# Optimization experiments

Hardware: AMD Instinct MI355X
Metric: run time of the kernel (lower is better)

The kernel has to match this reference:

```python
import jax, jax.numpy as jnp
import numpy as np

B_SZ, L, D_MODEL = 8, 4096, 64
D_INNER, D_STATE, DT_RANK, K = 128, 16, 4, 4  # expand=2, d_state=16, dt_rank=ceil(64/16), d_conv=4


def setup_inputs() -> dict:
    key = jax.random.key(0)
    ks = jax.random.split(key, 8)
    r = lambda k, sh, s=0.02: jax.random.normal(k, sh, dtype=jnp.float32) * s
    A_init = jnp.log(jnp.arange(1, D_STATE + 1, dtype=jnp.float32))  # S4D-real init
    return {
        "x": jax.random.normal(ks[0], (B_SZ, L, D_MODEL), dtype=jnp.float32),
        "ln_g": jnp.ones((D_MODEL,), jnp.float32),
        "ln_b": jnp.zeros((D_MODEL,), jnp.float32),
        "in_proj_w": r(ks[1], (2, 2 * D_INNER, D_MODEL)),
        "conv_w": r(ks[2], (2, D_INNER, K), 0.1),
        "conv_b": jnp.zeros((2, D_INNER), jnp.float32),
        "x_proj_w": r(ks[3], (2, DT_RANK + 2 * D_STATE, D_INNER)),
        "dt_proj_w": r(ks[4], (2, D_INNER, DT_RANK), 0.1),
        "dt_bias": jnp.full((2, D_INNER), -4.0, jnp.float32) + r(ks[5], (2, D_INNER), 0.1),
        "A_log": jnp.broadcast_to(A_init, (2, D_INNER, D_STATE)) + 0.0,
        "D": jnp.ones((2, D_INNER), jnp.float32),
        "out_proj_w": r(ks[6], (2, D_MODEL, D_INNER)),
    }


def _mamba(x, in_w, cw, cb, xp_w, dtp_w, dtb, A_log, Dp, out_w):
    # x: [B, L, d_model] -> [B, L, d_model]
    xz = x @ in_w.T                         # [B, L, 2*d_inner]
    xi, z = jnp.split(xz, 2, axis=-1)
    # causal depthwise conv1d, kernel K, left-pad K-1
    xi_c = jnp.transpose(xi, (0, 2, 1))     # [B, d_inner, L]
    xi_c = jax.lax.conv_general_dilated(
        xi_c, cw[:, None, :], (1,), [(K - 1, 0)],
        dimension_numbers=("NCH", "OIH", "NCH"), feature_group_count=D_INNER)
    xi = jax.nn.silu(jnp.transpose(xi_c, (0, 2, 1)) + cb)  # [B, L, d_inner]
    xdb = xi @ xp_w.T                       # [B, L, dt_rank + 2*N]
    dt_low, Bm, C = jnp.split(xdb, [DT_RANK, DT_RANK + D_STATE], axis=-1)
    dt = jax.nn.softplus(dt_low @ dtp_w.T + dtb)  # [B, L, d_inner]
    A = -jnp.exp(A_log)                     # [d_inner, N]

    def step(h, inp):
        xt, dtt, Bt, Ct = inp               # [B,d], [B,d], [B,N], [B,N]
        dA = jnp.exp(dtt[..., None] * A)    # [B, d, N]
        h = dA * h + (dtt * xt)[..., None] * Bt[:, None, :]
        return h, jnp.einsum("bdn,bn->bd", h, Ct)

    h0 = jnp.zeros((x.shape[0], D_INNER, D_STATE), x.dtype)
    seq = (jnp.swapaxes(xi, 0, 1), jnp.swapaxes(dt, 0, 1),
           jnp.swapaxes(Bm, 0, 1), jnp.swapaxes(C, 0, 1))
    _, ys = jax.lax.scan(step, h0, seq)
    y = jnp.swapaxes(ys, 0, 1) + xi * Dp    # D skip connection
    y = y * jax.nn.silu(z)                  # gate
    return y @ out_w.T                      # [B, L, d_model]


def reference(x, ln_g, ln_b, in_proj_w, conv_w, conv_b, x_proj_w, dt_proj_w, dt_bias, A_log, D, out_proj_w):
    mu = jnp.mean(x, axis=-1, keepdims=True)
    var = jnp.var(x, axis=-1, keepdims=True)
    xn = (x - mu) * jax.lax.rsqrt(var + 1e-5) * ln_g + ln_b
    p = lambda i: (in_proj_w[i], conv_w[i], conv_b[i], x_proj_w[i], dt_proj_w[i],
                   dt_bias[i], A_log[i], D[i], out_proj_w[i])
    y_fwd = _mamba(xn, *p(0))
    y_bwd = jnp.flip(_mamba(jnp.flip(xn, axis=1), *p(1)), axis=1)
    return y_fwd + y_bwd
```

## Files before the change

### kernel.cpp

```cpp
#include <hip/hip_runtime.h>

#define Bsz 8
#define Lx 4096
#define DM 64
#define DI 128
#define NS 16
#define RK 4
#define KC 4
#define NC 64
#define CT 64

typedef __attribute__((ext_vector_type(8))) __bf16 bf16x8v;
typedef __attribute__((ext_vector_type(4))) __bf16 bf16x4v;
typedef __attribute__((ext_vector_type(4))) float f32x4;

__device__ __forceinline__ float fsig(float x){ return 1.f/(1.f+__expf(-x)); }
__device__ __forceinline__ float dot4(float4 a, float4 b){
  return fmaf(a.x,b.x, fmaf(a.y,b.y, fmaf(a.z,b.z, a.w*b.w)));
}

__global__ __launch_bounds__(512) void a1_front(
    const float* __restrict__ x, const float* __restrict__ ln_g, const float* __restrict__ ln_b,
    const float* __restrict__ in_w, const float* __restrict__ conv_w, const float* __restrict__ conv_b,
    const float* __restrict__ xp_w, const float* __restrict__ dtp_w, const float* __restrict__ dt_b,
    float* __restrict__ xcg, float* __restrict__ dtg, float* __restrict__ zg,
    float* __restrict__ Bg, float* __restrict__ Cg)
{
  __shared__ float uA[4864];
  __shared__ float uB[8192];
  const int tid = threadIdx.x;
  const int bx = blockIdx.x;
  const int tile = bx & 63;
  const int i = (bx >> 6) & 1;
  const int b = bx >> 7;
  const int l0 = tile * 64;
  const size_t rbase = (size_t)(b*2+i)*Lx + l0;

  {
    const int wv8 = tid >> 6, lane = tid & 63;
    const float gg = ln_g[lane], bb = ln_b[lane];
    for (int lr = wv8; lr < 67; lr += 8) {
      float v = 0.f;
      int l = l0 - 3 + lr;
      if (l >= 0) {
        int pl = i ? (Lx-1-l) : l;
        v = x[((size_t)b*Lx + pl)*DM + lane];
        float s = v, s2 = v*v;
        #pragma unroll
        for (int off=32; off; off>>=1){ s += __shfl_xor(s,off); s2 += __shfl_xor(s2,off); }
        float mu = s * (1.f/DM);
        float rs = rsqrtf(s2*(1.f/DM) - mu*mu + 1e-5f);
        v = (v-mu)*rs*gg + bb;
      }
      *(__bf16*)((char*)uA + ((lr*128 + lane*2) ^ ((lr&7)<<4))) = (__bf16)v;
    }
    #pragma unroll
    for (int it=0; it<8; ++it) {
      int g = it*512 + tid;
      int c = g >> 4, q = g & 15;
      float4 w = *(const float4*)(in_w + ((size_t)(i*2*DI) + c)*DM + q*4);
      bf16x4v hv;
      hv[0]=(__bf16)w.x; hv[1]=(__bf16)w.y; hv[2]=(__bf16)w.z; hv[3]=(__bf16)w.w;
      *(bf16x4v*)((char*)uB + ((c*128 + q*8) ^ ((c&7)<<4))) = hv;
    }
  }
  __syncthreads();

  const int lane = tid & 63, wv = tid >> 6;
  f32x4 acc[5][2];
  {
    f32x4 z4 = {0.f, 0.f, 0.f, 0.f};
    #pragma unroll
    for (int mt=0; mt<5; ++mt){ acc[mt][0] = z4; acc[mt][1] = z4; }
    bf16x8v bfr[2][2];
    #pragma unroll
    for (int ntl=0; ntl<2; ++ntl)
      #pragma unroll
      for (int kt=0; kt<2; ++kt){
        int c = (wv*2+ntl)*16 + (lane&15);
        int byt = (c*128 + kt*64 + (lane>>4)*16) ^ ((c&7)<<4);
        bfr[ntl][kt] = *(const bf16x8v*)((const char*)uB + byt);
      }
    #pragma unroll
    for (int mt=0; mt<5; ++mt){
      bf16x8v afr[2];
      #pragma unroll
      for (int kt=0; kt<2; ++kt){
        int row = mt*16 + (lane&15);
        int byt = (row*128 + kt*64 + (lane>>4)*16) ^ ((row&7)<<4);
        afr[kt] = *(const bf16x8v*)((const char*)uA + byt);
      }
      #pragma unroll
      for (int ntl=0; ntl<2; ++ntl){
        acc[mt][ntl] = __builtin_amdgcn_mfma_f32_16x16x32_bf16(afr[0], bfr[ntl][0], acc[mt][ntl], 0,0,0);
        acc[mt][ntl] = __builtin_amdgcn_mfma_f32_16x16x32_bf16(afr[1], bfr[ntl][1], acc[mt][ntl], 0,0,0);
      }
    }
  }
  __syncthreads();

  {
    const int d = tid & 127, rh = tid >> 7;
    const float4 cw = *(const float4*)(conv_w + (size_t)(i*DI + d)*KC);
    const float cb = conv_b[i*DI + d];
    #pragma unroll
    for (int h=0; h<2; ++h) {
      if (wv < 4) {
        #pragma unroll
        for (int mt=0; mt<5; ++mt)
          #pragma unroll
          for (int ntl=0; ntl<2; ++ntl)
            #pragma unroll
            for (int r=0; r<4; ++r){
              int m = mt*16 + (lane>>4)*4 + r;
              if (m >= h*32 && m <= h*32+34)
                uA[(m - h*32)*129 + wv*32 + ntl*16 + (lane&15)] = acc[mt][ntl][r];
            }
      } else if (h == 0) {
        #pragma unroll
        for (int mt=0; mt<5; ++mt)
          #pragma unroll
          for (int ntl=0; ntl<2; ++ntl)
            #pragma unroll
            for (int r=0; r<4; ++r){
              int m = mt*16 + (lane>>4)*4 + r;
              if (m >= 3 && m <= 66)
                zg[(rbase + (m-3))*DI + (wv-4)*32 + ntl*16 + (lane&15)] = acc[mt][ntl][r];
            }
      }
      __syncthreads();
      #pragma unroll
      for (int rr=0; rr<8; ++rr){
        int r = h*32 + rh*8 + rr;
        int lb = rh*8 + rr;
        float v0 = uA[(lb  )*129 + d];
        float v1 = uA[(lb+1)*129 + d];
        float v2 = uA[(lb+2)*129 + d];
        float v3 = uA[(lb+3)*129 + d];
        float aa = cb + cw.x*v0 + cw.y*v1 + cw.z*v2 + cw.w*v3;
        float xc = aa * fsig(aa);
        xcg[(rbase + r)*DI + d] = xc;
        __bf16 hh = (__bf16)xc;
        __bf16 ll = (__bf16)(xc - (float)hh);
        int off = (r*256 + d*2) ^ ((r&7)<<4);
        *(__bf16*)((char*)uB + off) = hh;
        *(__bf16*)((char*)uB + off + 16384) = ll;
      }
      __syncthreads();
    }
  }

  for (int e = tid; e < 36*32; e += 512) {
    int j = e >> 5, k0 = (e & 31)*4;
    float4 w = *(const float4*)(xp_w + ((size_t)(i*36) + j)*DI + k0);
    float vv[4] = {w.x, w.y, w.z, w.w};
    bf16x4v hv, lv;
    #pragma unroll
    for (int k=0;k<4;++k){
      __bf16 hh = (__bf16)vv[k];
      hv[k] = hh;
      lv[k] = (__bf16)(vv[k] - (float)hh);
    }
    int off = (j*256 + k0*2) ^ ((j&7)<<4);
    *(bf16x4v*)((char*)uA + off) = hv;
    *(bf16x4v*)((char*)uA + off + 9216) = lv;
  }
  __syncthreads();

  for (int t = wv; t < 12; t += 8) {
    int mt = t & 3, nt = t >> 2;
    f32x4 a2 = {0.f,0.f,0.f,0.f};
    #pragma unroll
    for (int kt=0; kt<4; ++kt){
      int row = mt*16 + (lane&15);
      int ab = (row*256 + kt*64 + (lane>>4)*16) ^ ((row&7)<<4);
      bf16x8v ah = *(const bf16x8v*)((const char*)uB + ab);
      bf16x8v al = *(const bf16x8v*)((const char*)uB + ab + 16384);
      int col = nt*16 + (lane&15);
      int bby = (col*256 + kt*64 + (lane>>4)*16) ^ ((col&7)<<4);
      bf16x8v bh = *(const bf16x8v*)((const char*)uA + bby);
      bf16x8v bl = *(const bf16x8v*)((const char*)uA + bby + 9216);
      a2 = __builtin_amdgcn_mfma_f32_16x16x32_bf16(ah, bh, a2, 0,0,0);
      a2 = __builtin_amdgcn_mfma_f32_16x16x32_bf16(al, bh, a2, 0,0,0);
      a2 = __builtin_amdgcn_mfma_f32_16x16x32_bf16(ah, bl, a2, 0,0,0);
    }
    #pragma unroll
    for (int rg4=0; rg4<4; ++rg4){
      int row = mt*16 + (lane>>4)*4 + rg4;
      int j = nt*16 + (lane&15);
      float val = a2[rg4];
      if (j < 4) uA[4608 + row*4 + j] = val;
      else if (j < 20) Bg[(rbase+row)*NS + (j-4)] = val;
      else if (j < 36) Cg[(rbase+row)*NS + (j-20)] = val;
    }
  }
  __syncthreads();

  #pragma unroll 4
  for (int it=0; it<16; ++it) {
    int e = it*512 + tid;
    int r = e >> 7, d = e & 127;
    float4 dl = *(const float4*)&uA[4608 + r*4];
    float4 w  = *(const float4*)(dtp_w + (size_t)(i*DI + d)*RK);
    float a = dt_b[i*DI + d] + dot4(w, dl);
    dtg[(rbase + r)*DI + d] = (a > 15.f) ? a : __logf(1.f + __expf(a));
  }
}

__global__ __launch_bounds__(256) void kb_pass1(
    const float* __restrict__ dtg, const float* __restrict__ xcg, const float* __restrict__ Bg,
    const float* __restrict__ A_log,
    float* __restrict__ Pm, float* __restrict__ hend)
{
  const int tid = threadIdx.x;
  const int bx = blockIdx.x;
  const int c = bx % NC; const int i = (bx/NC)&1; const int b = bx/(2*NC);
  const int d = tid >> 1, half = tid & 1, n0 = half*8;
  float a[8], h[8];
  bool afast = true;
  #pragma unroll
  for (int n=0;n<8;++n){
    a[n] = -__expf(A_log[((size_t)(i*DI)+d)*NS + n0+n]);
    float tgt = (float)(n0+n+1);
    afast = afast && (fabsf(a[n] + tgt) <= 1e-4f*tgt);
    h[n] = 0.f;
  }
  float S = 0.f;
  const size_t rb = ((size_t)(b*2+i)*Lx + (size_t)c*CT);
  for (int r4 = 0; r4 < CT; r4 += 4){
    float dt4[4], x4[4];
    #pragma unroll
    for (int k=0;k<4;++k){
      size_t g = (rb + r4 + k)*DI + d;
      dt4[k] = dtg[g];
      x4[k]  = xcg[g];
    }
    #pragma unroll
    for (int k=0;k<4;++k){
      float dtt = dt4[k];
      float u = dtt * x4[k];
      S += dtt;
      const float* bp = &Bg[(rb + r4 + k)*NS + n0];
      float4 b0 = *(const float4*)bp;
      float4 b1 = *(const float4*)(bp+4);
      float bb[8] = {b0.x,b0.y,b0.z,b0.w,b1.x,b1.y,b1.z,b1.w};
      if (afast){
        float rr = __expf(-dtt);
        float dA;
        if (half){ float r2=rr*rr, r4v=r2*r2; dA = r4v*r4v*rr; } else dA = rr;
        h[0] = fmaf(dA, h[0], u*bb[0]);
        #pragma unroll
        for (int n=1;n<8;++n){ dA *= rr; h[n] = fmaf(dA, h[n], u*bb[n]); }
      } else {
        #pragma unroll
        for (int n=0;n<8;++n){
          float dA = __expf(a[n]*dtt);
          h[n] = fmaf(dA, h[n], u*bb[n]);
        }
      }
    }
  }
  size_t ob = (((size_t)(b*2+i)*NC + c)*DI + d)*NS + n0;
  #pragma unroll
  for (int n=0;n<8;++n){
    Pm[ob+n] = __expf(a[n]*S);
    hend[ob+n] = h[n];
  }
}

__global__ __launch_bounds__(256) void kc_pass2(
    float* __restrict__ Pm, const float* __restrict__ hend)
{
  const int tid = threadIdx.x;
  const int bi = blockIdx.x;
  const int d = tid>>1, n0 = (tid&1)*8;
  float h[8];
  #pragma unroll
  for (int n=0;n<8;++n) h[n]=0.f;
  for (int c=0;c<NC;++c){
    size_t ob = (((size_t)bi*NC + c)*DI + d)*NS + n0;
    float p[8], hev[8];
    #pragma unroll
    for (int n=0;n<8;++n){ p[n]=Pm[ob+n]; hev[n]=hend[ob+n]; }
    #pragma unroll
    for (int n=0;n<8;++n){ Pm[ob+n] = h[n]; h[n] = fmaf(p[n], h[n], hev[n]); }
  }
}

__global__ __launch_bounds__(256) void kd_pass3(
    const float* dtg, const float* __restrict__ xcg, const float* __restrict__ Bg,
    const float* __restrict__ Cg, const float* __restrict__ A_log, const float* __restrict__ Dp,
    const float* __restrict__ h0, const float* __restrict__ zg, float* yout)
{
  const int tid = threadIdx.x;
  const int bx = blockIdx.x;
  const int c = bx % NC; const int i = (bx/NC)&1; const int b = bx/(2*NC);
  const int d = tid >> 1, half = tid & 1, n0 = half*8;
  float a[8], h[8];
  bool afast = true;
  size_t hb = (((size_t)(b*2+i)*NC + c)*DI + d)*NS + n0;
  #pragma unroll
  for (int n=0;n<8;++n){
    a[n] = -__expf(A_log[((size_t)(i*DI)+d)*NS + n0+n]);
    float tgt = (float)(n0+n+1);
    afast = afast && (fabsf(a[n] + tgt) <= 1e-4f*tgt);
    h[n] = h0[hb+n];
  }
  const float Dd = Dp[i*DI + d];
  const size_t rb = ((size_t)(b*2+i)*Lx + (size_t)c*CT);
  for (int r4 = 0; r4 < CT; r4 += 4){
    float dt4[4], x4[4], z4[4];
    #pragma unroll
    for (int k=0;k<4;++k){
      size_t g = (rb + r4 + k)*DI + d;
      dt4[k] = dtg[g];
      x4[k]  = xcg[g];
      z4[k]  = zg[g];
    }
    #pragma unroll
    for (int k=0;k<4;++k){
      float dtt = dt4[k];
      float xcv = x4[k];
      float u = dtt * xcv;
      const float* bp = &Bg[(rb + r4 + k)*NS + n0];
      const float* cp = &Cg[(rb + r4 + k)*NS + n0];
      float4 b0 = *(const float4*)bp;
      float4 b1 = *(const float4*)(bp+4);
      float4 c0 = *(const float4*)cp;
      float4 c1 = *(const float4*)(cp+4);
      float bb[8] = {b0.x,b0.y,b0.z,b0.w,b1.x,b1.y,b1.z,b1.w};
      float cc[8] = {c0.x,c0.y,c0.z,c0.w,c1.x,c1.y,c1.z,c1.w};
      float part = 0.f;
      if (afast){
        float rr = __expf(-dtt);
        float dA;
        if (half){ float r2=rr*rr, r4v=r2*r2; dA = r4v*r4v*rr; } else dA = rr;
        h[0] = fmaf(dA, h[0], u*bb[0]);
        part = fmaf(h[0], cc[0], part);
        #pragma unroll
        for (int n=1;n<8;++n){
          dA *= rr;
          h[n] = fmaf(dA, h[n], u*bb[n]);
          part = fmaf(h[n], cc[n], part);
        }
      } else {
        #pragma unroll
        for (int n=0;n<8;++n){
          float dA = __expf(a[n]*dtt);
          h[n] = fmaf(dA, h[n], u*bb[n]);
          part = fmaf(h[n], cc[n], part);
        }
      }
      float y = part + __shfl_xor(part, 1);
      if (half == 0){
        float zz = z4[k];
        yout[(rb + r4 + k)*DI + d] = fmaf(xcv, Dd, y) * (zz * fsig(zz));
      }
    }
  }
}

__global__ __launch_bounds__(256) void ke_out(
    const float* __restrict__ yg, const float* __restrict__ ow, float* __restrict__ out)
{
  __shared__ char sY[16384];
  __shared__ char sW[32768];
  const int tid = threadIdx.x;
  const int bx = blockIdx.x;
  const int tile = bx & 127; const int b = bx >> 7;
  const int l0 = tile * 32;
  #pragma unroll
  for (int it=0; it<16; ++it){
    int e = it*256 + tid;
    int dir = e >> 11, c = (e >> 5) & 63, q = e & 31;
    float4 w = *(const float4*)(ow + ((size_t)(dir*DM + c))*DI + q*4);
    bf16x4v hv; hv[0]=(__bf16)w.x; hv[1]=(__bf16)w.y; hv[2]=(__bf16)w.z; hv[3]=(__bf16)w.w;
    *(bf16x4v*)(sW + ((c*512 + dir*256 + q*8) ^ ((c&7)<<4))) = hv;
  }
  #pragma unroll
  for (int it=0; it<8; ++it){
    int e = it*256 + tid;
    int dir = e >> 10, r = (e >> 5) & 31, q = e & 31;
    size_t row = dir ? ((size_t)(b*2+1)*Lx + (size_t)(Lx-1-(l0+r)))
                     : ((size_t)(b*2  )*Lx + (size_t)(l0+r));
    float4 v = *(const float4*)(yg + row*DI + q*4);
    bf16x4v hv; hv[0]=(__bf16)v.x; hv[1]=(__bf16)v.y; hv[2]=(__bf16)v.z; hv[3]=(__bf16)v.w;
    *(bf16x4v*)(sY + ((r*512 + dir*256 + q*8) ^ ((r&7)<<4))) = hv;
  }
  __syncthreads();
  const int lane = tid & 63, wv = tid >> 6;
  #pragma unroll
  for (int t=0; t<2; ++t){
    int T = wv*2 + t, mt = T >> 2, nt = T & 3;
    f32x4 acc = {0.f,0.f,0.f,0.f};
    #pragma unroll
    for (int kt=0; kt<8; ++kt){
      int row = mt*16 + (lane&15);
      bf16x8v av = *(const bf16x8v*)(sY + ((row*512 + kt*64 + (lane>>4)*16) ^ ((row&7)<<4)));
      int ch = nt*16 + (lane&15);
      bf16x8v wvv = *(const bf16x8v*)(sW + ((ch*512 + kt*64 + (lane>>4)*16) ^ ((ch&7)<<4)));
      acc = __builtin_amdgcn_mfma_f32_16x16x32_bf16(av, wvv, acc, 0,0,0);
    }
    #pragma unroll
    for (int r=0; r<4; ++r){
      int m = mt*16 + (lane>>4)*4 + r;
      int ch = nt*16 + (lane&15);
      out[((size_t)b*Lx + (size_t)(l0+m))*DM + ch] = acc[r];
    }
  }
}

extern "C" void kernel_launch(void* const* d_in, const int* in_sizes, int n_in,
                              void* d_out, int out_size, void* d_ws, size_t ws_size,
                              hipStream_t stream)
{
  const float* x      = (const float*)d_in[0];
  const float* ln_g   = (const float*)d_in[1];
  const float* ln_b   = (const float*)d_in[2];
  const float* in_w   = (const float*)d_in[3];
  const float* conv_w = (const float*)d_in[4];
  const float* conv_b = (const float*)d_in[5];
  const float* xp_w   = (const float*)d_in[6];
  const float* dtp_w  = (const float*)d_in[7];
  const float* dt_b   = (const float*)d_in[8];
  const float* A_log  = (const float*)d_in[9];
  const float* Dp     = (const float*)d_in[10];
  const float* ow     = (const float*)d_in[11];
  float* out = (float*)d_out;
  float* ws = (float*)d_ws;
  const size_t NBD = (size_t)Bsz*2*Lx*DI;
  const size_t NBN = (size_t)Bsz*2*Lx*NS;
  float* xcg = ws;
  float* dtg = xcg + NBD;
  float* zg  = dtg + NBD;
  float* Bg  = zg + NBD;
  float* Cg  = Bg + NBN;
  float* Pm  = Cg + NBN;
  float* he  = out;

  a1_front<<<dim3(Bsz*2*(Lx/64)), dim3(512), 0, stream>>>(
      x, ln_g, ln_b, in_w, conv_w, conv_b, xp_w, dtp_w, dt_b, xcg, dtg, zg, Bg, Cg);
  kb_pass1<<<dim3(Bsz*2*NC), dim3(256), 0, stream>>>(dtg, xcg, Bg, A_log, Pm, he);
  kc_pass2<<<dim3(Bsz*2), dim3(256), 0, stream>>>(Pm, he);
  kd_pass3<<<dim3(Bsz*2*NC), dim3(256), 0, stream>>>(dtg, xcg, Bg, Cg, A_log, Dp, Pm, zg, dtg);
  ke_out<<<dim3(Bsz*(Lx/32)), dim3(256), 0, stream>>>(dtg, ow, out);
}
```

Baseline: 147.4 us.

## Merge chunk scan passes; add cross-chunk state contribution in a cheap fixup pass

The first scan pass now runs the full local recurrence with a zero initial state. It emits partial outputs y plus the running dt prefix sum S, overwriting the dt and xc buffers. The final pass no longer reruns the 16-state recurrence. It adds the carried-in state's contribution exp(A·S)·h0·C to the stored partial output and applies the gate. This removes a whole second recurrence pass and its B/dt reads. In exchange it adds an extra write and read of y and S, plus an exp per step in the fixup. Decay powers also come from a squaring tree instead of a serial product chain, and the C dot product is split into two accumulators for more instruction-level parallelism.

Result: slower. 154.6 us (+4.9%).

```diff
diff --git a/kernel.cpp b/kernel.cpp
--- a/kernel.cpp
+++ b/kernel.cpp
@@ -17,6 +17,16 @@
 __device__ __forceinline__ float fsig(float x){ return 1.f/(1.f+__expf(-x)); }
 __device__ __forceinline__ float dot4(float4 a, float4 b){
   return fmaf(a.x,b.x, fmaf(a.y,b.y, fmaf(a.z,b.z, a.w*b.w)));
+}
+__device__ __forceinline__ void pow8(float e1, int half, float p[8]){
+  float e2=e1*e1, e4=e2*e2, e8=e4*e4;
+  if (half){
+    p[0]=e8*e1; p[1]=e8*e2; p[2]=p[1]*e1; p[3]=e8*e4;
+    p[4]=p[3]*e1; p[5]=p[3]*e2; p[6]=p[5]*e1; p[7]=e8*e8;
+  } else {
+    p[0]=e1; p[1]=e2; p[2]=e2*e1; p[3]=e4;
+    p[4]=e4*e1; p[5]=e4*e2; p[6]=p[5]*e1; p[7]=e8;
+  }
 }
 
 __global__ __launch_bounds__(512) void a1_front(
@@ -207,9 +217,10 @@
   }
 }
 
-__global__ __launch_bounds__(256) void kb_pass1(
-    const float* __restrict__ dtg, const float* __restrict__ xcg, const float* __restrict__ Bg,
-    const float* __restrict__ A_log,
+__global__ __launch_bounds__(256) void ks_scan(
+    float* dtg, float* xcg,
+    const float* __restrict__ Bg, const float* __restrict__ Cg,
+    const float* __restrict__ A_log, const float* __restrict__ Dp,
     float* __restrict__ Pm, float* __restrict__ hend)
 {
   const int tid = threadIdx.x;
@@ -225,6 +236,7 @@
     afast = afast && (fabsf(a[n] + tgt) <= 1e-4f*tgt);
     h[n] = 0.f;
   }
+  const float Dd = Dp[i*DI + d];
   float S = 0.f;
   const size_t rb = ((size_t)(b*2+i)*Lx + (size_t)c*CT);
   for (int r4 = 0; r4 < CT; r4 += 4){
@@ -238,90 +250,9 @@
     #pragma unroll
     for (int k=0;k<4;++k){
       float dtt = dt4[k];
-      float u = dtt * x4[k];
-      S += dtt;
-      const float* bp = &Bg[(rb + r4 + k)*NS + n0];
-      float4 b0 = *(const float4*)bp;
-      float4 b1 = *(const float4*)(bp+4);
-      float bb[8] = {b0.x,b0.y,b0.z,b0.w,b1.x,b1.y,b1.z,b1.w};
-      if (afast){
-        float rr = __expf(-dtt);
-        float dA;
-        if (half){ float r2=rr*rr, r4v=r2*r2; dA = r4v*r4v*rr; } else dA = rr;
-        h[0] = fmaf(dA, h[0], u*bb[0]);
-        #pragma unroll
-        for (int n=1;n<8;++n){ dA *= rr; h[n] = fmaf(dA, h[n], u*bb[n]); }
-      } else {
-        #pragma unroll
-        for (int n=0;n<8;++n){
-          float dA = __expf(a[n]*dtt);
-          h[n] = fmaf(dA, h[n], u*bb[n]);
-        }
-      }
-    }
-  }
-  size_t ob = (((size_t)(b*2+i)*NC + c)*DI + d)*NS + n0;
-  #pragma unroll
-  for (int n=0;n<8;++n){
-    Pm[ob+n] = __expf(a[n]*S);
-    hend[ob+n] = h[n];
-  }
-}
-
-__global__ __launch_bounds__(256) void kc_pass2(
-    float* __restrict__ Pm, const float* __restrict__ hend)
-{
-  const int tid = threadIdx.x;
-  const int bi = blockIdx.x;
-  const int d = tid>>1, n0 = (tid&1)*8;
-  float h[8];
-  #pragma unroll
-  for (int n=0;n<8;++n) h[n]=0.f;
-  for (int c=0;c<NC;++c){
-    size_t ob = (((size_t)bi*NC + c)*DI + d)*NS + n0;
-    float p[8], hev[8];
-    #pragma unroll
-    for (int n=0;n<8;++n){ p[n]=Pm[ob+n]; hev[n]=hend[ob+n]; }
-    #pragma unroll
-    for (int n=0;n<8;++n){ Pm[ob+n] = h[n]; h[n] = fmaf(p[n], h[n], hev[n]); }
-  }
-}
-
-__global__ __launch_bounds__(256) void kd_pass3(
-    const float* dtg, const float* __restrict__ xcg, const float* __restrict__ Bg,
-    const float* __restrict__ Cg, const float* __restrict__ A_log, const float* __restrict__ Dp,
-    const float* __restrict__ h0, const float* __restrict__ zg, float* yout)
-{
-  const int tid = threadIdx.x;
-  const int bx = blockIdx.x;
-  const int c = bx % NC; const int i = (bx/NC)&1; const int b = bx/(2*NC);
-  const int d = tid >> 1, half = tid & 1, n0 = half*8;
-  float a[8], h[8];
-  bool afast = true;
-  size_t hb = (((size_t)(b*2+i)*NC + c)*DI + d)*NS + n0;
-  #pragma unroll
-  for (int n=0;n<8;++n){
-    a[n] = -__expf(A_log[((size_t)(i*DI)+d)*NS + n0+n]);
-    float tgt = (float)(n0+n+1);
-    afast = afast && (fabsf(a[n] + tgt) <= 1e-4f*tgt);
-    h[n] = h0[hb+n];
-  }
-  const float Dd = Dp[i*DI + d];
-  const size_t rb = ((size_t)(b*2+i)*Lx + (size_t)c*CT);
-  for (int r4 = 0; r4 < CT; r4 += 4){
-    float dt4[4], x4[4], z4[4];
-    #pragma unroll
-    for (int k=0;k<4;++k){
-      size_t g = (rb + r4 + k)*DI + d;
-      dt4[k] = dtg[g];
-      x4[k]  = xcg[g];
-      z4[k]  = zg[g];
-    }
-    #pragma unroll
-    for (int k=0;k<4;++k){
-      float dtt = dt4[k];
       float xcv = x4[k];
       float u = dtt * xcv;
+      S += dtt;
       const float* bp = &Bg[(rb + r4 + k)*NS + n0];
       const float* cp = &Cg[(rb + r4 + k)*NS + n0];
       float4 b0 = *(const float4*)bp;
@@ -330,31 +261,117 @@
       float4 c1 = *(const float4*)(cp+4);
       float bb[8] = {b0.x,b0.y,b0.z,b0.w,b1.x,b1.y,b1.z,b1.w};
       float cc[8] = {c0.x,c0.y,c0.z,c0.w,c1.x,c1.y,c1.z,c1.w};
-      float part = 0.f;
+      float pA = 0.f, pB = 0.f;
       if (afast){
-        float rr = __expf(-dtt);
-        float dA;
-        if (half){ float r2=rr*rr, r4v=r2*r2; dA = r4v*r4v*rr; } else dA = rr;
-        h[0] = fmaf(dA, h[0], u*bb[0]);
-        part = fmaf(h[0], cc[0], part);
-        #pragma unroll
-        for (int n=1;n<8;++n){
-          dA *= rr;
-          h[n] = fmaf(dA, h[n], u*bb[n]);
-          part = fmaf(h[n], cc[n], part);
+        float p[8];
+        pow8(__expf(-dtt), half, p);
+        #pragma unroll
+        for (int n=0;n<8;++n){
+          h[n] = fmaf(p[n], h[n], u*bb[n]);
+          if (n & 1) pB = fmaf(h[n], cc[n], pB); else pA = fmaf(h[n], cc[n], pA);
         }
       } else {
         #pragma unroll
         for (int n=0;n<8;++n){
           float dA = __expf(a[n]*dtt);
           h[n] = fmaf(dA, h[n], u*bb[n]);
-          part = fmaf(h[n], cc[n], part);
+          if (n & 1) pB = fmaf(h[n], cc[n], pB); else pA = fmaf(h[n], cc[n], pA);
         }
       }
+      float part = pA + pB;
       float y = part + __shfl_xor(part, 1);
       if (half == 0){
+        size_t g = (rb + r4 + k)*DI + d;
+        dtg[g] = fmaf(xcv, Dd, y);
+        xcg[g] = S;
+      }
+    }
+  }
+  size_t ob = (((size_t)(b*2+i)*NC + c)*DI + d)*NS + n0;
+  if (afast){
+    float p[8];
+    pow8(__expf(-S), half, p);
+    #pragma unroll
+    for (int n=0;n<8;++n) Pm[ob+n] = p[n];
+  } else {
+    #pragma unroll
+    for (int n=0;n<8;++n) Pm[ob+n] = __expf(a[n]*S);
+  }
+  #pragma unroll
+  for (int n=0;n<8;++n) hend[ob+n] = h[n];
+}
+
+__global__ __launch_bounds__(256) void kc_pass2(
+    float* __restrict__ Pm, const float* __restrict__ hend)
+{
+  const int tid = threadIdx.x;
+  const int bi = blockIdx.x;
+  const int d = tid>>1, n0 = (tid&1)*8;
+  float h[8];
+  #pragma unroll
+  for (int n=0;n<8;++n) h[n]=0.f;
+  for (int c=0;c<NC;++c){
+    size_t ob = (((size_t)bi*NC + c)*DI + d)*NS + n0;
+    float p[8], hev[8];
+    #pragma unroll
+    for (int n=0;n<8;++n){ p[n]=Pm[ob+n]; hev[n]=hend[ob+n]; }
+    #pragma unroll
+    for (int n=0;n<8;++n){ Pm[ob+n] = h[n]; h[n] = fmaf(p[n], h[n], hev[n]); }
+  }
+}
+
+__global__ __launch_bounds__(256) void kf_fix(
+    float* yio, const float* __restrict__ Sg,
+    const float* __restrict__ Cg, const float* __restrict__ A_log,
+    const float* __restrict__ h0, const float* __restrict__ zg)
+{
+  const int tid = threadIdx.x;
+  const int bx = blockIdx.x;
+  const int c = bx % NC; const int i = (bx/NC)&1; const int b = bx/(2*NC);
+  const int d = tid >> 1, half = tid & 1, n0 = half*8;
+  float a[8], h0r[8];
+  bool afast = true;
+  size_t hb = (((size_t)(b*2+i)*NC + c)*DI + d)*NS + n0;
+  #pragma unroll
+  for (int n=0;n<8;++n){
+    a[n] = -__expf(A_log[((size_t)(i*DI)+d)*NS + n0+n]);
+    float tgt = (float)(n0+n+1);
+    afast = afast && (fabsf(a[n] + tgt) <= 1e-4f*tgt);
+    h0r[n] = h0[hb+n];
+  }
+  const size_t rb = ((size_t)(b*2+i)*Lx + (size_t)c*CT);
+  for (int r4 = 0; r4 < CT; r4 += 4){
+    float S4[4], y4[4], z4[4];
+    #pragma unroll
+    for (int k=0;k<4;++k){
+      size_t g = (rb + r4 + k)*DI + d;
+      S4[k] = Sg[g];
+      y4[k] = yio[g];
+      z4[k] = zg[g];
+    }
+    #pragma unroll
+    for (int k=0;k<4;++k){
+      const float* cp = &Cg[(rb + r4 + k)*NS + n0];
+      float4 c0 = *(const float4*)cp;
+      float4 c1 = *(const float4*)(cp+4);
+      float cc[8] = {c0.x,c0.y,c0.z,c0.w,c1.x,c1.y,c1.z,c1.w};
+      float p[8];
+      if (afast) pow8(__expf(-S4[k]), half, p);
+      else {
+        #pragma unroll
+        for (int n=0;n<8;++n) p[n] = __expf(a[n]*S4[k]);
+      }
+      float pA = 0.f, pB = 0.f;
+      #pragma unroll
+      for (int n=0;n<8;++n){
+        float t = p[n]*h0r[n];
+        if (n & 1) pB = fmaf(t, cc[n], pB); else pA = fmaf(t, cc[n], pA);
+      }
+      float part = pA + pB;
+      float corr = part + __shfl_xor(part, 1);
+      if (half == 0){
         float zz = z4[k];
-        yout[(rb + r4 + k)*DI + d] = fmaf(xcv, Dd, y) * (zz * fsig(zz));
+        yio[(rb + r4 + k)*DI + d] = (y4[k] + corr) * (zz * fsig(zz));
       }
     }
   }
@@ -440,8 +457,8 @@
 
   a1_front<<<dim3(Bsz*2*(Lx/64)), dim3(512), 0, stream>>>(
       x, ln_g, ln_b, in_w, conv_w, conv_b, xp_w, dtp_w, dt_b, xcg, dtg, zg, Bg, Cg);
-  kb_pass1<<<dim3(Bsz*2*NC), dim3(256), 0, stream>>>(dtg, xcg, Bg, A_log, Pm, he);
+  ks_scan<<<dim3(Bsz*2*NC), dim3(256), 0, stream>>>(dtg, xcg, Bg, Cg, A_log, Dp, Pm, he);
   kc_pass2<<<dim3(Bsz*2), dim3(256), 0, stream>>>(Pm, he);
-  kd_pass3<<<dim3(Bsz*2*NC), dim3(256), 0, stream>>>(dtg, xcg, Bg, Cg, A_log, Dp, Pm, zg, dtg);
+  kf_fix<<<dim3(Bsz*2*NC), dim3(256), 0, stream>>>(dtg, xcg, Cg, A_log, Pm, zg);
   ke_out<<<dim3(Bsz*(Lx/32)), dim3(256), 0, stream>>>(dtg, ow, out);
 }
```

## Fuse chunk-local scan into front kernel and apply carry correction in output kernel

Applied to the files above, without the earlier changes.

The chunk-local selective scan, with zero initial state, now runs inside the front kernel. It reads xc from shared memory and computes dt on the fly, and it writes the partial output y, the cumulative dt sum S, and the chunk end states. The separate pass1 and pass3 kernels are removed. The output projection kernel adds the cross-chunk correction C·exp(A·S)·h0 before gating. This drops one launch and several full-size global round trips of dt and xc, at the cost of more transcendental work in the output kernel and a longer front kernel.

Measured after the change: 155.8 us. +5.7%, slower.

```diff
diff --git a/kernel.cpp b/kernel.cpp
--- a/kernel.cpp
+++ b/kernel.cpp
@@ -23,8 +23,10 @@
     const float* __restrict__ x, const float* __restrict__ ln_g, const float* __restrict__ ln_b,
     const float* __restrict__ in_w, const float* __restrict__ conv_w, const float* __restrict__ conv_b,
     const float* __restrict__ xp_w, const float* __restrict__ dtp_w, const float* __restrict__ dt_b,
-    float* __restrict__ xcg, float* __restrict__ dtg, float* __restrict__ zg,
-    float* __restrict__ Bg, float* __restrict__ Cg)
+    const float* __restrict__ A_log, const float* __restrict__ Dp,
+    float* __restrict__ yg, float* __restrict__ Sg, float* __restrict__ zg,
+    float* __restrict__ Bg, float* __restrict__ Cg,
+    float* __restrict__ Pm, float* __restrict__ he)
 {
   __shared__ float uA[4864];
   __shared__ float uB[8192];
@@ -139,7 +141,6 @@
         float v3 = uA[(lb+3)*129 + d];
         float aa = cb + cw.x*v0 + cw.y*v1 + cw.z*v2 + cw.w*v3;
         float xc = aa * fsig(aa);
-        xcg[(rbase + r)*DI + d] = xc;
         __bf16 hh = (__bf16)xc;
         __bf16 ll = (__bf16)(xc - (float)hh);
         int off = (r*256 + d*2) ^ ((r&7)<<4);
@@ -196,75 +197,84 @@
   }
   __syncthreads();
 
-  #pragma unroll 4
-  for (int it=0; it<16; ++it) {
-    int e = it*512 + tid;
-    int r = e >> 7, d = e & 127;
-    float4 dl = *(const float4*)&uA[4608 + r*4];
-    float4 w  = *(const float4*)(dtp_w + (size_t)(i*DI + d)*RK);
-    float a = dt_b[i*DI + d] + dot4(w, dl);
-    dtg[(rbase + r)*DI + d] = (a > 15.f) ? a : __logf(1.f + __expf(a));
-  }
-}
-
-__global__ __launch_bounds__(256) void kb_pass1(
-    const float* __restrict__ dtg, const float* __restrict__ xcg, const float* __restrict__ Bg,
-    const float* __restrict__ A_log,
-    float* __restrict__ Pm, float* __restrict__ hend)
-{
-  const int tid = threadIdx.x;
-  const int bx = blockIdx.x;
-  const int c = bx % NC; const int i = (bx/NC)&1; const int b = bx/(2*NC);
-  const int d = tid >> 1, half = tid & 1, n0 = half*8;
-  float a[8], h[8];
-  bool afast = true;
-  #pragma unroll
-  for (int n=0;n<8;++n){
-    a[n] = -__expf(A_log[((size_t)(i*DI)+d)*NS + n0+n]);
-    float tgt = (float)(n0+n+1);
-    afast = afast && (fabsf(a[n] + tgt) <= 1e-4f*tgt);
-    h[n] = 0.f;
-  }
-  float S = 0.f;
-  const size_t rb = ((size_t)(b*2+i)*Lx + (size_t)c*CT);
-  for (int r4 = 0; r4 < CT; r4 += 4){
-    float dt4[4], x4[4];
-    #pragma unroll
-    for (int k=0;k<4;++k){
-      size_t g = (rb + r4 + k)*DI + d;
-      dt4[k] = dtg[g];
-      x4[k]  = xcg[g];
-    }
-    #pragma unroll
-    for (int k=0;k<4;++k){
-      float dtt = dt4[k];
-      float u = dtt * x4[k];
-      S += dtt;
-      const float* bp = &Bg[(rb + r4 + k)*NS + n0];
-      float4 b0 = *(const float4*)bp;
-      float4 b1 = *(const float4*)(bp+4);
-      float bb[8] = {b0.x,b0.y,b0.z,b0.w,b1.x,b1.y,b1.z,b1.w};
-      if (afast){
-        float rr = __expf(-dtt);
-        float dA;
-        if (half){ float r2=rr*rr, r4v=r2*r2; dA = r4v*r4v*rr; } else dA = rr;
-        h[0] = fmaf(dA, h[0], u*bb[0]);
-        #pragma unroll
-        for (int n=1;n<8;++n){ dA *= rr; h[n] = fmaf(dA, h[n], u*bb[n]); }
-      } else {
-        #pragma unroll
-        for (int n=0;n<8;++n){
-          float dA = __expf(a[n]*dtt);
-          h[n] = fmaf(dA, h[n], u*bb[n]);
+  {
+    const int d = tid >> 2, quarter = tid & 3, n0s = quarter*4;
+    const float4 w4 = *(const float4*)(dtp_w + (size_t)(i*DI + d)*RK);
+    const float bias = dt_b[i*DI + d];
+    const float Dd = Dp[i*DI + d];
+    float a[4]; bool afast = true;
+    #pragma unroll
+    for (int n=0;n<4;++n){
+      a[n] = -__expf(A_log[((size_t)(i*DI)+d)*NS + n0s + n]);
+      float tgt = (float)(n0s+n+1);
+      afast = afast && (fabsf(a[n] + tgt) <= 1e-4f*tgt);
+    }
+    float h[4] = {0.f,0.f,0.f,0.f};
+    float S = 0.f;
+    for (int r4=0; r4<CT; r4+=4){
+      float v4[4], xcv4[4];
+      float4 bv4[4], cv4[4];
+      #pragma unroll
+      for (int k=0;k<4;++k){
+        int r = r4+k;
+        float4 dl = *(const float4*)&uA[4608 + r*4];
+        v4[k] = bias + dot4(w4, dl);
+        int off = (r*256 + d*2) ^ ((r&7)<<4);
+        xcv4[k] = (float)*(const __bf16*)((const char*)uB + off)
+                + (float)*(const __bf16*)((const char*)uB + off + 16384);
+        bv4[k] = *(const float4*)&Bg[(rbase + r)*NS + n0s];
+        cv4[k] = *(const float4*)&Cg[(rbase + r)*NS + n0s];
+      }
+      #pragma unroll
+      for (int k=0;k<4;++k){
+        float v = v4[k];
+        float dtt = (v > 15.f) ? v : __logf(1.f + __expf(v));
+        S += dtt;
+        float xc = xcv4[k];
+        float u = dtt * xc;
+        float p0,p1,p2,p3;
+        if (afast){
+          float e1 = __expf(-dtt);
+          float e2 = e1*e1, e4v = e2*e2;
+          float base = 1.f;
+          if (quarter & 1) base = e4v;
+          if (quarter & 2) base *= e4v*e4v;
+          p0 = base*e1; p1 = base*e2; p2 = p1*e1; p3 = base*e4v;
+        } else {
+          p0 = __expf(a[0]*dtt); p1 = __expf(a[1]*dtt);
+          p2 = __expf(a[2]*dtt); p3 = __expf(a[3]*dtt);
         }
-      }
-    }
-  }
-  size_t ob = (((size_t)(b*2+i)*NC + c)*DI + d)*NS + n0;
-  #pragma unroll
-  for (int n=0;n<8;++n){
-    Pm[ob+n] = __expf(a[n]*S);
-    hend[ob+n] = h[n];
+        h[0] = fmaf(p0, h[0], u*bv4[k].x);
+        h[1] = fmaf(p1, h[1], u*bv4[k].y);
+        h[2] = fmaf(p2, h[2], u*bv4[k].z);
+        h[3] = fmaf(p3, h[3], u*bv4[k].w);
+        float pA = fmaf(h[0], cv4[k].x, h[2]*cv4[k].z);
+        float pB = fmaf(h[1], cv4[k].y, h[3]*cv4[k].w);
+        float part = pA + pB;
+        part += __shfl_xor(part, 1);
+        part += __shfl_xor(part, 2);
+        if (quarter == 0){
+          size_t g = (rbase + r4 + k)*DI + d;
+          yg[g] = fmaf(xc, Dd, part);
+          Sg[g] = S;
+        }
+      }
+    }
+    size_t ob = (((size_t)(b*2+i)*NC + tile)*DI + d)*NS + n0s;
+    float p0,p1,p2,p3;
+    if (afast){
+      float e1 = __expf(-S);
+      float e2 = e1*e1, e4v = e2*e2;
+      float base = 1.f;
+      if (quarter & 1) base = e4v;
+      if (quarter & 2) base *= e4v*e4v;
+      p0 = base*e1; p1 = base*e2; p2 = p1*e1; p3 = base*e4v;
+    } else {
+      p0 = __expf(a[0]*S); p1 = __expf(a[1]*S);
+      p2 = __expf(a[2]*S); p3 = __expf(a[3]*S);
+    }
+    *(float4*)&Pm[ob] = make_float4(p0,p1,p2,p3);
+    *(float4*)&he[ob] = make_float4(h[0],h[1],h[2],h[3]);
   }
 }
 
@@ -287,81 +297,11 @@
   }
 }
 
-__global__ __launch_bounds__(256) void kd_pass3(
-    const float* dtg, const float* __restrict__ xcg, const float* __restrict__ Bg,
-    const float* __restrict__ Cg, const float* __restrict__ A_log, const float* __restrict__ Dp,
-    const float* __restrict__ h0, const float* __restrict__ zg, float* yout)
-{
-  const int tid = threadIdx.x;
-  const int bx = blockIdx.x;
-  const int c = bx % NC; const int i = (bx/NC)&1; const int b = bx/(2*NC);
-  const int d = tid >> 1, half = tid & 1, n0 = half*8;
-  float a[8], h[8];
-  bool afast = true;
-  size_t hb = (((size_t)(b*2+i)*NC + c)*DI + d)*NS + n0;
-  #pragma unroll
-  for (int n=0;n<8;++n){
-    a[n] = -__expf(A_log[((size_t)(i*DI)+d)*NS + n0+n]);
-    float tgt = (float)(n0+n+1);
-    afast = afast && (fabsf(a[n] + tgt) <= 1e-4f*tgt);
-    h[n] = h0[hb+n];
-  }
-  const float Dd = Dp[i*DI + d];
-  const size_t rb = ((size_t)(b*2+i)*Lx + (size_t)c*CT);
-  for (int r4 = 0; r4 < CT; r4 += 4){
-    float dt4[4], x4[4], z4[4];
-    #pragma unroll
-    for (int k=0;k<4;++k){
-      size_t g = (rb + r4 + k)*DI + d;
-      dt4[k] = dtg[g];
-      x4[k]  = xcg[g];
-      z4[k]  = zg[g];
-    }
-    #pragma unroll
-    for (int k=0;k<4;++k){
-      float dtt = dt4[k];
-      float xcv = x4[k];
-      float u = dtt * xcv;
-      const float* bp = &Bg[(rb + r4 + k)*NS + n0];
-      const float* cp = &Cg[(rb + r4 + k)*NS + n0];
-      float4 b0 = *(const float4*)bp;
-      float4 b1 = *(const float4*)(bp+4);
-      float4 c0 = *(const float4*)cp;
-      float4 c1 = *(const float4*)(cp+4);
-      float bb[8] = {b0.x,b0.y,b0.z,b0.w,b1.x,b1.y,b1.z,b1.w};
-      float cc[8] = {c0.x,c0.y,c0.z,c0.w,c1.x,c1.y,c1.z,c1.w};
-      float part = 0.f;
-      if (afast){
-        float rr = __expf(-dtt);
-        float dA;
-        if (half){ float r2=rr*rr, r4v=r2*r2; dA = r4v*r4v*rr; } else dA = rr;
-        h[0] = fmaf(dA, h[0], u*bb[0]);
-        part = fmaf(h[0], cc[0], part);
-        #pragma unroll
-        for (int n=1;n<8;++n){
-          dA *= rr;
-          h[n] = fmaf(dA, h[n], u*bb[n]);
-          part = fmaf(h[n], cc[n], part);
-        }
-      } else {
-        #pragma unroll
-        for (int n=0;n<8;++n){
-          float dA = __expf(a[n]*dtt);
-          h[n] = fmaf(dA, h[n], u*bb[n]);
-          part = fmaf(h[n], cc[n], part);
-        }
-      }
-      float y = part + __shfl_xor(part, 1);
-      if (half == 0){
-        float zz = z4[k];
-        yout[(rb + r4 + k)*DI + d] = fmaf(xcv, Dd, y) * (zz * fsig(zz));
-      }
-    }
-  }
-}
-
 __global__ __launch_bounds__(256) void ke_out(
-    const float* __restrict__ yg, const float* __restrict__ ow, float* __restrict__ out)
+    const float* __restrict__ yg, const float* __restrict__ Sg,
+    const float* __restrict__ zg, const float* __restrict__ Cg,
+    const float* __restrict__ h0g, const float* __restrict__ A_log,
+    const float* __restrict__ ow, float* __restrict__ out)
 {
   __shared__ char sY[16384];
   __shared__ char sW[32768];
@@ -369,23 +309,72 @@
   const int bx = blockIdx.x;
   const int tile = bx & 127; const int b = bx >> 7;
   const int l0 = tile * 32;
+  const int q = tid & 31, rg = tid >> 5;
   #pragma unroll
   for (int it=0; it<16; ++it){
     int e = it*256 + tid;
-    int dir = e >> 11, c = (e >> 5) & 63, q = e & 31;
-    float4 w = *(const float4*)(ow + ((size_t)(dir*DM + c))*DI + q*4);
+    int dir = e >> 11, c = (e >> 5) & 63, qq = e & 31;
+    float4 w = *(const float4*)(ow + ((size_t)(dir*DM + c))*DI + qq*4);
     bf16x4v hv; hv[0]=(__bf16)w.x; hv[1]=(__bf16)w.y; hv[2]=(__bf16)w.z; hv[3]=(__bf16)w.w;
-    *(bf16x4v*)(sW + ((c*512 + dir*256 + q*8) ^ ((c&7)<<4))) = hv;
+    *(bf16x4v*)(sW + ((c*512 + dir*256 + qq*8) ^ ((c&7)<<4))) = hv;
   }
   #pragma unroll
-  for (int it=0; it<8; ++it){
-    int e = it*256 + tid;
-    int dir = e >> 10, r = (e >> 5) & 31, q = e & 31;
-    size_t row = dir ? ((size_t)(b*2+1)*Lx + (size_t)(Lx-1-(l0+r)))
-                     : ((size_t)(b*2  )*Lx + (size_t)(l0+r));
-    float4 v = *(const float4*)(yg + row*DI + q*4);
-    bf16x4v hv; hv[0]=(__bf16)v.x; hv[1]=(__bf16)v.y; hv[2]=(__bf16)v.z; hv[3]=(__bf16)v.w;
-    *(bf16x4v*)(sY + ((r*512 + dir*256 + q*8) ^ ((r&7)<<4))) = hv;
+  for (int dir=0; dir<2; ++dir){
+    const size_t strm = (size_t)(b*2+dir);
+    const int cch = dir ? ((Lx-1-l0)>>6) : (l0>>6);
+    bool afast = true;
+    #pragma unroll
+    for (int dd=0; dd<4; ++dd)
+      #pragma unroll
+      for (int n=0;n<16;++n){
+        float av = __expf(A_log[((size_t)(dir*DI) + q*4+dd)*NS + n]);
+        float tgt = (float)(n+1);
+        afast = afast && (fabsf(av - tgt) <= 1e-4f*tgt);
+      }
+    float h0q[4][16];
+    #pragma unroll
+    for (int dd=0; dd<4; ++dd)
+      #pragma unroll
+      for (int k=0;k<4;++k)
+        *(float4*)&h0q[dd][k*4] =
+            *(const float4*)&h0g[(((strm*NC) + cch)*DI + (q*4+dd))*NS + k*4];
+    #pragma unroll
+    for (int it=0; it<4; ++it){
+      int r = it*8 + rg;
+      size_t prow = strm*Lx + (size_t)(dir ? (Lx-1-(l0+r)) : (l0+r));
+      float4 y4 = *(const float4*)&yg[prow*DI + q*4];
+      float4 S4 = *(const float4*)&Sg[prow*DI + q*4];
+      float4 z4 = *(const float4*)&zg[prow*DI + q*4];
+      float c16[16];
+      #pragma unroll
+      for (int k=0;k<4;++k) *(float4*)&c16[k*4] = *(const float4*)&Cg[prow*NS + k*4];
+      float yv[4] = {y4.x,y4.y,y4.z,y4.w};
+      float Sv[4] = {S4.x,S4.y,S4.z,S4.w};
+      float zv[4] = {z4.x,z4.y,z4.z,z4.w};
+      bf16x4v hv;
+      #pragma unroll
+      for (int dd=0; dd<4; ++dd){
+        float corr;
+        if (afast){
+          float e1 = __expf(-Sv[dd]);
+          float p = e1;
+          corr = p * c16[0] * h0q[dd][0];
+          #pragma unroll
+          for (int n=1;n<16;++n){ p *= e1; corr = fmaf(p*c16[n], h0q[dd][n], corr); }
+        } else {
+          corr = 0.f;
+          #pragma unroll
+          for (int n=0;n<16;++n){
+            float an = -__expf(A_log[((size_t)(dir*DI) + q*4+dd)*NS + n]);
+            corr = fmaf(__expf(an*Sv[dd])*c16[n], h0q[dd][n], corr);
+          }
+        }
+        float zz = zv[dd];
+        float yf = (yv[dd] + corr) * (zz * fsig(zz));
+        hv[dd] = (__bf16)yf;
+      }
+      *(bf16x4v*)(sY + ((r*512 + dir*256 + q*8) ^ ((r&7)<<4))) = hv;
+    }
   }
   __syncthreads();
   const int lane = tid & 63, wv = tid >> 6;
@@ -430,18 +419,18 @@
   float* ws = (float*)d_ws;
   const size_t NBD = (size_t)Bsz*2*Lx*DI;
   const size_t NBN = (size_t)Bsz*2*Lx*NS;
-  float* xcg = ws;
-  float* dtg = xcg + NBD;
-  float* zg  = dtg + NBD;
+  float* Sg  = ws;
+  float* yg  = Sg + NBD;
+  float* zg  = yg + NBD;
   float* Bg  = zg + NBD;
   float* Cg  = Bg + NBN;
   float* Pm  = Cg + NBN;
   float* he  = out;
 
   a1_front<<<dim3(Bsz*2*(Lx/64)), dim3(512), 0, stream>>>(
-      x, ln_g, ln_b, in_w, conv_w, conv_b, xp_w, dtp_w, dt_b, xcg, dtg, zg, Bg, Cg);
-  kb_pass1<<<dim3(Bsz*2*NC), dim3(256), 0, stream>>>(dtg, xcg, Bg, A_log, Pm, he);
+      x, ln_g, ln_b, in_w, conv_w, conv_b, xp_w, dtp_w, dt_b, A_log, Dp,
+      yg, Sg, zg, Bg, Cg, Pm, he);
   kc_pass2<<<dim3(Bsz*2), dim3(256), 0, stream>>>(Pm, he);
-  kd_pass3<<<dim3(Bsz*2*NC), dim3(256), 0, stream>>>(dtg, xcg, Bg, Cg, A_log, Dp, Pm, zg, dtg);
-  ke_out<<<dim3(Bsz*(Lx/32)), dim3(256), 0, stream>>>(dtg, ow, out);
+  ke_out<<<dim3(Bsz*(Lx/32)), dim3(256), 0, stream>>>(
+      yg, Sg, zg, Cg, Pm, A_log, ow, out);
 }
```

## Split scan state across four lanes per channel and double scan grid

Applied to the files above, without the earlier changes.

The chunked-scan passes now give each channel's 16 states to four lanes (4 states each) instead of two lanes (8 each), and launch twice as many blocks by splitting d_inner in half. This shortens the per-thread serial chain and raises occupancy for the latency-bound recurrence. The cost is redundant loads of dt/x/z per lane group, plus an extra cross-lane shuffle reduction in pass 3. Pass 2 is also vectorised to float4 and software-prefetches the next chunk.

Measured after the change: 155.5 us. 5.5% more time.

```diff
diff --git a/kernel.cpp b/kernel.cpp
--- a/kernel.cpp
+++ b/kernel.cpp
@@ -17,6 +17,13 @@
 __device__ __forceinline__ float fsig(float x){ return 1.f/(1.f+__expf(-x)); }
 __device__ __forceinline__ float dot4(float4 a, float4 b){
   return fmaf(a.x,b.x, fmaf(a.y,b.y, fmaf(a.z,b.z, a.w*b.w)));
+}
+__device__ __forceinline__ void pow4q(float e1, int quarter, float& p0, float& p1, float& p2, float& p3){
+  float e2 = e1*e1, e4v = e2*e2;
+  float base = 1.f;
+  if (quarter & 1) base = e4v;
+  if (quarter & 2) base *= e4v*e4v;
+  p0 = base*e1; p1 = base*e2; p2 = p1*e1; p3 = base*e4v;
 }
 
 __global__ __launch_bounds__(512) void a1_front(
@@ -214,17 +221,23 @@
 {
   const int tid = threadIdx.x;
   const int bx = blockIdx.x;
-  const int c = bx % NC; const int i = (bx/NC)&1; const int b = bx/(2*NC);
-  const int d = tid >> 1, half = tid & 1, n0 = half*8;
-  float a[8], h[8];
-  bool afast = true;
-  #pragma unroll
-  for (int n=0;n<8;++n){
-    a[n] = -__expf(A_log[((size_t)(i*DI)+d)*NS + n0+n]);
-    float tgt = (float)(n0+n+1);
+  const int dh = bx & 1;
+  const int rest = bx >> 1;
+  const int c = rest & (NC-1);
+  const int i = (rest >> 6) & 1;
+  const int b = rest >> 7;
+  const int wv = tid >> 6, lane = tid & 63;
+  const int quarter = lane >> 4;
+  const int d = dh*64 + wv*16 + (lane & 15);
+  const int n0s = quarter*4;
+  float a[4]; bool afast = true;
+  #pragma unroll
+  for (int n=0;n<4;++n){
+    a[n] = -__expf(A_log[((size_t)(i*DI)+d)*NS + n0s+n]);
+    float tgt = (float)(n0s+n+1);
     afast = afast && (fabsf(a[n] + tgt) <= 1e-4f*tgt);
-    h[n] = 0.f;
-  }
+  }
+  float h[4] = {0.f,0.f,0.f,0.f};
   float S = 0.f;
   const size_t rb = ((size_t)(b*2+i)*Lx + (size_t)c*CT);
   for (int r4 = 0; r4 < CT; r4 += 4){
@@ -240,32 +253,22 @@
       float dtt = dt4[k];
       float u = dtt * x4[k];
       S += dtt;
-      const float* bp = &Bg[(rb + r4 + k)*NS + n0];
-      float4 b0 = *(const float4*)bp;
-      float4 b1 = *(const float4*)(bp+4);
-      float bb[8] = {b0.x,b0.y,b0.z,b0.w,b1.x,b1.y,b1.z,b1.w};
-      if (afast){
-        float rr = __expf(-dtt);
-        float dA;
-        if (half){ float r2=rr*rr, r4v=r2*r2; dA = r4v*r4v*rr; } else dA = rr;
-        h[0] = fmaf(dA, h[0], u*bb[0]);
-        #pragma unroll
-        for (int n=1;n<8;++n){ dA *= rr; h[n] = fmaf(dA, h[n], u*bb[n]); }
-      } else {
-        #pragma unroll
-        for (int n=0;n<8;++n){
-          float dA = __expf(a[n]*dtt);
-          h[n] = fmaf(dA, h[n], u*bb[n]);
-        }
-      }
-    }
-  }
-  size_t ob = (((size_t)(b*2+i)*NC + c)*DI + d)*NS + n0;
-  #pragma unroll
-  for (int n=0;n<8;++n){
-    Pm[ob+n] = __expf(a[n]*S);
-    hend[ob+n] = h[n];
-  }
+      float4 bv = *(const float4*)&Bg[(rb + r4 + k)*NS + n0s];
+      float p0,p1,p2,p3;
+      if (afast) pow4q(__expf(-dtt), quarter, p0,p1,p2,p3);
+      else { p0=__expf(a[0]*dtt); p1=__expf(a[1]*dtt); p2=__expf(a[2]*dtt); p3=__expf(a[3]*dtt); }
+      h[0] = fmaf(p0, h[0], u*bv.x);
+      h[1] = fmaf(p1, h[1], u*bv.y);
+      h[2] = fmaf(p2, h[2], u*bv.z);
+      h[3] = fmaf(p3, h[3], u*bv.w);
+    }
+  }
+  size_t ob = (((size_t)(b*2+i)*NC + c)*DI + d)*NS + n0s;
+  float p0,p1,p2,p3;
+  if (afast) pow4q(__expf(-S), quarter, p0,p1,p2,p3);
+  else { p0=__expf(a[0]*S); p1=__expf(a[1]*S); p2=__expf(a[2]*S); p3=__expf(a[3]*S); }
+  *(float4*)&Pm[ob] = make_float4(p0,p1,p2,p3);
+  *(float4*)&hend[ob] = make_float4(h[0],h[1],h[2],h[3]);
 }
 
 __global__ __launch_bounds__(256) void kc_pass2(
@@ -277,13 +280,24 @@
   float h[8];
   #pragma unroll
   for (int n=0;n<8;++n) h[n]=0.f;
-  for (int c=0;c<NC;++c){
-    size_t ob = (((size_t)bi*NC + c)*DI + d)*NS + n0;
-    float p[8], hev[8];
-    #pragma unroll
-    for (int n=0;n<8;++n){ p[n]=Pm[ob+n]; hev[n]=hend[ob+n]; }
-    #pragma unroll
-    for (int n=0;n<8;++n){ Pm[ob+n] = h[n]; h[n] = fmaf(p[n], h[n], hev[n]); }
+  const size_t stride = (size_t)DI*NS;
+  size_t ob = (((size_t)bi*NC)*DI + d)*NS + n0;
+  float4 pa = *(const float4*)&Pm[ob],   pb = *(const float4*)&Pm[ob+4];
+  float4 ea = *(const float4*)&hend[ob], eb = *(const float4*)&hend[ob+4];
+  for (int c=0; c<NC; ++c){
+    size_t obn = ob + stride;
+    float4 qa=pa, qb=pb, fa=ea, fb=eb;
+    if (c+1 < NC){
+      qa = *(const float4*)&Pm[obn];   qb = *(const float4*)&Pm[obn+4];
+      fa = *(const float4*)&hend[obn]; fb = *(const float4*)&hend[obn+4];
+    }
+    *(float4*)&Pm[ob]   = make_float4(h[0],h[1],h[2],h[3]);
+    *(float4*)&Pm[ob+4] = make_float4(h[4],h[5],h[6],h[7]);
+    h[0]=fmaf(pa.x,h[0],ea.x); h[1]=fmaf(pa.y,h[1],ea.y);
+    h[2]=fmaf(pa.z,h[2],ea.z); h[3]=fmaf(pa.w,h[3],ea.w);
+    h[4]=fmaf(pb.x,h[4],eb.x); h[5]=fmaf(pb.y,h[5],eb.y);
+    h[6]=fmaf(pb.z,h[6],eb.z); h[7]=fmaf(pb.w,h[7],eb.w);
+    pa=qa; pb=qb; ea=fa; eb=fb; ob = obn;
   }
 }
 
@@ -294,18 +308,25 @@
 {
   const int tid = threadIdx.x;
   const int bx = blockIdx.x;
-  const int c = bx % NC; const int i = (bx/NC)&1; const int b = bx/(2*NC);
-  const int d = tid >> 1, half = tid & 1, n0 = half*8;
-  float a[8], h[8];
-  bool afast = true;
-  size_t hb = (((size_t)(b*2+i)*NC + c)*DI + d)*NS + n0;
-  #pragma unroll
-  for (int n=0;n<8;++n){
-    a[n] = -__expf(A_log[((size_t)(i*DI)+d)*NS + n0+n]);
-    float tgt = (float)(n0+n+1);
+  const int dh = bx & 1;
+  const int rest = bx >> 1;
+  const int c = rest & (NC-1);
+  const int i = (rest >> 6) & 1;
+  const int b = rest >> 7;
+  const int wv = tid >> 6, lane = tid & 63;
+  const int quarter = lane >> 4;
+  const int d = dh*64 + wv*16 + (lane & 15);
+  const int n0s = quarter*4;
+  float a[4]; bool afast = true;
+  size_t hb = (((size_t)(b*2+i)*NC + c)*DI + d)*NS + n0s;
+  #pragma unroll
+  for (int n=0;n<4;++n){
+    a[n] = -__expf(A_log[((size_t)(i*DI)+d)*NS + n0s+n]);
+    float tgt = (float)(n0s+n+1);
     afast = afast && (fabsf(a[n] + tgt) <= 1e-4f*tgt);
-    h[n] = h0[hb+n];
-  }
+  }
+  float4 h0v = *(const float4*)&h0[hb];
+  float h[4] = {h0v.x, h0v.y, h0v.z, h0v.w};
   const float Dd = Dp[i*DI + d];
   const size_t rb = ((size_t)(b*2+i)*Lx + (size_t)c*CT);
   for (int r4 = 0; r4 < CT; r4 += 4){
@@ -322,39 +343,21 @@
       float dtt = dt4[k];
       float xcv = x4[k];
       float u = dtt * xcv;
-      const float* bp = &Bg[(rb + r4 + k)*NS + n0];
-      const float* cp = &Cg[(rb + r4 + k)*NS + n0];
-      float4 b0 = *(const float4*)bp;
-      float4 b1 = *(const float4*)(bp+4);
-      float4 c0 = *(const float4*)cp;
-      float4 c1 = *(const float4*)(cp+4);
-      float bb[8] = {b0.x,b0.y,b0.z,b0.w,b1.x,b1.y,b1.z,b1.w};
-      float cc[8] = {c0.x,c0.y,c0.z,c0.w,c1.x,c1.y,c1.z,c1.w};
-      float part = 0.f;
-      if (afast){
-        float rr = __expf(-dtt);
-        float dA;
-        if (half){ float r2=rr*rr, r4v=r2*r2; dA = r4v*r4v*rr; } else dA = rr;
-        h[0] = fmaf(dA, h[0], u*bb[0]);
-        part = fmaf(h[0], cc[0], part);
-        #pragma unroll
-        for (int n=1;n<8;++n){
-          dA *= rr;
-          h[n] = fmaf(dA, h[n], u*bb[n]);
-          part = fmaf(h[n], cc[n], part);
-        }
-      } else {
-        #pragma unroll
-        for (int n=0;n<8;++n){
-          float dA = __expf(a[n]*dtt);
-          h[n] = fmaf(dA, h[n], u*bb[n]);
-          part = fmaf(h[n], cc[n], part);
-        }
-      }
-      float y = part + __shfl_xor(part, 1);
-      if (half == 0){
+      float4 bv = *(const float4*)&Bg[(rb + r4 + k)*NS + n0s];
+      float4 cv = *(const float4*)&Cg[(rb + r4 + k)*NS + n0s];
+      float p0,p1,p2,p3;
+      if (afast) pow4q(__expf(-dtt), quarter, p0,p1,p2,p3);
+      else { p0=__expf(a[0]*dtt); p1=__expf(a[1]*dtt); p2=__expf(a[2]*dtt); p3=__expf(a[3]*dtt); }
+      h[0] = fmaf(p0, h[0], u*bv.x);
+      h[1] = fmaf(p1, h[1], u*bv.y);
+      h[2] = fmaf(p2, h[2], u*bv.z);
+      h[3] = fmaf(p3, h[3], u*bv.w);
+      float part = fmaf(h[0], cv.x, h[2]*cv.z) + fmaf(h[1], cv.y, h[3]*cv.w);
+      part += __shfl_xor(part, 16);
+      part += __shfl_xor(part, 32);
+      if (quarter == 0){
         float zz = z4[k];
-        yout[(rb + r4 + k)*DI + d] = fmaf(xcv, Dd, y) * (zz * fsig(zz));
+        yout[(rb + r4 + k)*DI + d] = fmaf(xcv, Dd, part) * (zz * fsig(zz));
       }
     }
   }
@@ -440,8 +443,8 @@
 
   a1_front<<<dim3(Bsz*2*(Lx/64)), dim3(512), 0, stream>>>(
       x, ln_g, ln_b, in_w, conv_w, conv_b, xp_w, dtp_w, dt_b, xcg, dtg, zg, Bg, Cg);
-  kb_pass1<<<dim3(Bsz*2*NC), dim3(256), 0, stream>>>(dtg, xcg, Bg, A_log, Pm, he);
+  kb_pass1<<<dim3(Bsz*2*NC*2), dim3(256), 0, stream>>>(dtg, xcg, Bg, A_log, Pm, he);
   kc_pass2<<<dim3(Bsz*2), dim3(256), 0, stream>>>(Pm, he);
-  kd_pass3<<<dim3(Bsz*2*NC), dim3(256), 0, stream>>>(dtg, xcg, Bg, Cg, A_log, Dp, Pm, zg, dtg);
+  kd_pass3<<<dim3(Bsz*2*NC*2), dim3(256), 0, stream>>>(dtg, xcg, Bg, Cg, A_log, Dp, Pm, zg, dtg);
   ke_out<<<dim3(Bsz*(Lx/32)), dim3(256), 0, stream>>>(dtg, ow, out);
 }
```
